# Optimization experiments

Hardware: AMD Instinct MI355X
Metric: run time of the kernel (lower is better)

Reference implementation:

```python
import jax, jax.numpy as jnp
import numpy as np

EPS = 1e-6

def rmsnorm(x, w):
    rms = jnp.sqrt(jnp.mean(x * x, axis=-1, keepdims=True) + EPS)
    return w * x / rms

def setup_inputs() -> dict:
    key = jax.random.key(0)
    ks = jax.random.split(key, 12)
    B, L, D, S, E, H = 2, 2048, 1024, 16, 4, 2048
    x = jax.random.normal(ks[0], (B, L, D), jnp.float32)
    A_log = jnp.log(jax.random.uniform(ks[1], (D, S), jnp.float32) * 0.5 + 0.5)
    D_param = jnp.ones((D,), jnp.float32)
    W_delta = jax.random.normal(ks[2], (D, D), jnp.float32) * 0.02
    b_delta = jnp.zeros((D,), jnp.float32)
    W_B = jax.random.normal(ks[3], (D, S), jnp.float32) * 0.02
    W_C = jax.random.normal(ks[4], (D, S), jnp.float32) * 0.02
    W_router = jax.random.normal(ks[5], (D, E), jnp.float32) * 0.02
    Wg = jax.random.normal(ks[6], (E, D, H), jnp.float32) * 0.02
    Wu = jax.random.normal(ks[7], (E, D, H), jnp.float32) * 0.02
    Wd = jax.random.normal(ks[8], (E, H, D), jnp.float32) * 0.02
    wn_exp = jnp.ones((E, H), jnp.float32)
    norm_w = jnp.ones((D,), jnp.float32)
    return dict(x=x, A_log=A_log, D_param=D_param, W_delta=W_delta, b_delta=b_delta,
                W_B=W_B, W_C=W_C, W_router=W_router, Wg=Wg, Wu=Wu, Wd=Wd,
                wn_exp=wn_exp, norm_w=norm_w)

def reference(x, A_log, D_param, W_delta, b_delta, W_B, W_C, W_router, Wg, Wu, Wd, wn_exp, norm_w):
    B, L, D = x.shape
    # input-dependent SSM parameters
    delta = jax.nn.softplus(x @ W_delta + b_delta)        # (B,L,D)
    Bm = x @ W_B                                          # (B,L,S)
    Cm = x @ W_C                                          # (B,L,S)
    A = -jnp.exp(A_log)                                   # (D,S)
    S = A.shape[1]
    h0 = jnp.zeros((B, D, S), x.dtype)
    xs = (jnp.moveaxis(x, 1, 0), jnp.moveaxis(delta, 1, 0),
          jnp.moveaxis(Bm, 1, 0), jnp.moveaxis(Cm, 1, 0))

    def step(h, inp):
        x_t, d_t, B_t, C_t = inp                          # (B,D),(B,D),(B,S),(B,S)
        bar_A = jnp.exp(jnp.minimum(d_t[..., None] * A, 10.0))          # (B,D,S)
        bar_B = jnp.clip(d_t[..., None] * B_t[:, None, :], -10.0, 10.0)  # (B,D,S)
        h = jnp.clip(bar_A * h + bar_B * x_t[..., None], -10000.0, 10000.0)
        y_t = jnp.sum(h * C_t[:, None, :], axis=-1) + x_t * D_param     # (B,D)
        return h, y_t

    _, ys = jax.lax.scan(step, h0, xs)                    # ys: (L,B,D)
    ssm_out = jnp.moveaxis(ys, 0, 1)                      # (B,L,D)

    # top-2 MoE over flattened tokens
    flat = ssm_out.reshape(-1, D)                         # (N,D)
    probs = jax.nn.softmax(flat @ W_router, axis=-1)      # (N,E)
    w2, idx2 = jax.lax.top_k(probs, 2)
    w2 = w2 / (jnp.sum(w2, axis=-1, keepdims=True) + 1e-9)

    def expert(xf, wg, wu, wd, wn):
        g = jax.nn.silu(xf @ wg) * (xf @ wu)
        g = rmsnorm(g, wn)
        return g @ wd

    all_out = jax.vmap(expert, in_axes=(None, 0, 0, 0, 0))(flat, Wg, Wu, Wd, wn_exp)  # (E,N,D)
    tok = jnp.arange(flat.shape[0])
    moe = (w2[:, 0, None] * all_out[idx2[:, 0], tok]
           + w2[:, 1, None] * all_out[idx2[:, 1], tok])   # (N,D)

    out = rmsnorm(ssm_out + moe.reshape(B, L, D), norm_w)
    return out  # dropout is identity in eval mode
```

## Files before the change

kernel.cpp:

```cpp
#include <hip/hip_runtime.h>
#include <hip/hip_bf16.h>


typedef __bf16 bfrag __attribute__((ext_vector_type(8)));
typedef float f32x4 __attribute__((ext_vector_type(4)));

constexpr int Ddim = 1024;
constexpr int Sdim = 16;
constexpr int Eexp = 4;
constexpr int Hdim = 2048;
constexpr int Lseq = 2048;
constexpr int Bb   = 2;
constexpr int Ntok = 4096;
constexpr int NC   = 32;
constexpr int CL   = 64;
constexpr int DG   = 64;

__device__ __forceinline__ float softplus_f(float z) {
  return z > 20.f ? z : log1pf(__expf(z));
}

__device__ __forceinline__ bfrag cvt8(float4 a, float4 b) {
  bfrag r;
  r[0] = (__bf16)a.x; r[1] = (__bf16)a.y; r[2] = (__bf16)a.z; r[3] = (__bf16)a.w;
  r[4] = (__bf16)b.x; r[5] = (__bf16)b.y; r[6] = (__bf16)b.z; r[7] = (__bf16)b.w;
  return r;
}

__device__ __forceinline__ void cvt8_split(float4 a, float4 b, bfrag& h, bfrag& l) {
  float v[8] = {a.x, a.y, a.z, a.w, b.x, b.y, b.z, b.w};
  #pragma unroll
  for (int k = 0; k < 8; k++) {
    __bf16 hh = (__bf16)v[k];
    h[k] = hh;
    l[k] = (__bf16)(v[k] - (float)hh);
  }
}

__device__ __forceinline__ void gload16(const void* g, void* l) {
  __builtin_amdgcn_global_load_lds(
      (const __attribute__((address_space(1))) void*)g,
      (__attribute__((address_space(3))) void*)l, 16, 0, 0);
}

__global__ __launch_bounds__(256) void tr_cvt(const float* __restrict__ src,
                                              __bf16* __restrict__ dst,
                                              int R, int C) {
  __shared__ float tile[32][33];
  const size_t boff = (size_t)blockIdx.z * R * C;
  const int c0 = blockIdx.x * 32, r0 = blockIdx.y * 32;
  const int tx = threadIdx.x & 31, ty = threadIdx.x >> 5;
  #pragma unroll
  for (int i = 0; i < 4; i++)
    tile[ty + 8 * i][tx] = src[boff + (size_t)(r0 + ty + 8 * i) * C + c0 + tx];
  __syncthreads();
  #pragma unroll
  for (int i = 0; i < 4; i++)
    dst[boff + (size_t)(c0 + ty + 8 * i) * R + r0 + tx] = (__bf16)tile[tx][ty + 8 * i];
}

__global__ __launch_bounds__(256) void tr_split(const float* __restrict__ src,
                                                __bf16* __restrict__ dhi,
                                                __bf16* __restrict__ dlo,
                                                int R, int C) {
  __shared__ float tile[32][33];
  const size_t boff = (size_t)blockIdx.z * R * C;
  const int c0 = blockIdx.x * 32, r0 = blockIdx.y * 32;
  const int tx = threadIdx.x & 31, ty = threadIdx.x >> 5;
  #pragma unroll
  for (int i = 0; i < 4; i++)
    tile[ty + 8 * i][tx] = src[boff + (size_t)(r0 + ty + 8 * i) * C + c0 + tx];
  __syncthreads();
  #pragma unroll
  for (int i = 0; i < 4; i++) {
    float v = tile[tx][ty + 8 * i];
    __bf16 h = (__bf16)v;
    size_t idx = boff + (size_t)(c0 + ty + 8 * i) * R + r0 + tx;
    dhi[idx] = h;
    dlo[idx] = (__bf16)(v - (float)h);
  }
}

__global__ __launch_bounds__(256) void cvt_bf(const float* __restrict__ s,
                                              __bf16* __restrict__ d) {
  const size_t i = ((size_t)blockIdx.x * 256 + threadIdx.x) * 8;
  float4 f0 = *(const float4*)&s[i];
  float4 f1 = *(const float4*)&s[i + 4];
  *(bfrag*)&d[i] = cvt8(f0, f1);
}

__global__ __launch_bounds__(256) void cvt_xsplit(const float* __restrict__ s,
                                                  __bf16* __restrict__ dh,
                                                  __bf16* __restrict__ dl) {
  const size_t i = ((size_t)blockIdx.x * 256 + threadIdx.x) * 8;
  float4 f0 = *(const float4*)&s[i];
  float4 f1 = *(const float4*)&s[i + 4];
  bfrag h, l;
  cvt8_split(f0, f1, h, l);
  *(bfrag*)&dh[i] = h;
  *(bfrag*)&dl[i] = l;
}

__global__ __launch_bounds__(256) void gemm_delta(
    const __bf16* __restrict__ xh, const __bf16* __restrict__ xl,
    const __bf16* __restrict__ Bhi, const __bf16* __restrict__ Blo,
    const float* __restrict__ bias, float* __restrict__ outp) {
  const int n0 = blockIdx.x * 128;
  const int m0 = blockIdx.y * 128;
  const int t = threadIdx.x;
  const int lane = t & 63;
  const int w = t >> 6;
  const int wm = w >> 1, wn = w & 1;
  const int lr = lane & 15, kq = lane >> 4;

  __shared__ __attribute__((aligned(16))) __bf16 Ah[128 * 32];
  __shared__ __attribute__((aligned(16))) __bf16 Al[128 * 32];
  __shared__ __attribute__((aligned(16))) __bf16 Bh[128 * 32];
  __shared__ __attribute__((aligned(16))) __bf16 Bl[128 * 32];

  f32x4 acc[4][4];
  const f32x4 z4 = {0.f, 0.f, 0.f, 0.f};
  #pragma unroll
  for (int i = 0; i < 4; i++)
    #pragma unroll
    for (int j = 0; j < 4; j++) acc[i][j] = z4;

  const int sr0 = (w * 2 + 0) * 16 + (lane >> 2);
  const int sr1 = (w * 2 + 1) * 16 + (lane >> 2);
  const int skc = (lane & 3) * 8;
  const __bf16* ah0 = xh + (size_t)(m0 + sr0) * Ddim + skc;
  const __bf16* ah1 = xh + (size_t)(m0 + sr1) * Ddim + skc;
  const __bf16* al0 = xl + (size_t)(m0 + sr0) * Ddim + skc;
  const __bf16* al1 = xl + (size_t)(m0 + sr1) * Ddim + skc;
  const __bf16* bh0 = Bhi + (size_t)(n0 + sr0) * Ddim + skc;
  const __bf16* bh1 = Bhi + (size_t)(n0 + sr1) * Ddim + skc;
  const __bf16* bl0 = Blo + (size_t)(n0 + sr0) * Ddim + skc;
  const __bf16* bl1 = Blo + (size_t)(n0 + sr1) * Ddim + skc;
  __bf16* lAh0 = &Ah[(w * 2 + 0) * 512];
  __bf16* lAh1 = &Ah[(w * 2 + 1) * 512];
  __bf16* lAl0 = &Al[(w * 2 + 0) * 512];
  __bf16* lAl1 = &Al[(w * 2 + 1) * 512];
  __bf16* lBh0 = &Bh[(w * 2 + 0) * 512];
  __bf16* lBh1 = &Bh[(w * 2 + 1) * 512];
  __bf16* lBl0 = &Bl[(w * 2 + 0) * 512];
  __bf16* lBl1 = &Bl[(w * 2 + 1) * 512];

  for (int k0 = 0; k0 < Ddim; k0 += 32) {
    __syncthreads();
    gload16(ah0 + k0, lAh0); gload16(ah1 + k0, lAh1);
    gload16(al0 + k0, lAl0); gload16(al1 + k0, lAl1);
    gload16(bh0 + k0, lBh0); gload16(bh1 + k0, lBh1);
    gload16(bl0 + k0, lBl0); gload16(bl1 + k0, lBl1);
    __syncthreads();
    bfrag ah[4], al_[4], bh[4], bl[4];
    #pragma unroll
    for (int i = 0; i < 4; i++) {
      const int off = (wm * 64 + i * 16 + lr) * 32 + kq * 8;
      ah[i] = *(const bfrag*)&Ah[off];
      al_[i] = *(const bfrag*)&Al[off];
    }
    #pragma unroll
    for (int j = 0; j < 4; j++) {
      const int off = (wn * 64 + j * 16 + lr) * 32 + kq * 8;
      bh[j] = *(const bfrag*)&Bh[off];
      bl[j] = *(const bfrag*)&Bl[off];
    }
    #pragma unroll
    for (int i = 0; i < 4; i++)
      #pragma unroll
      for (int j = 0; j < 4; j++) {
        f32x4 tacc = acc[i][j];
        tacc = __builtin_amdgcn_mfma_f32_16x16x32_bf16(al_[i], bl[j], tacc, 0, 0, 0);
        tacc = __builtin_amdgcn_mfma_f32_16x16x32_bf16(ah[i], bl[j], tacc, 0, 0, 0);
        tacc = __builtin_amdgcn_mfma_f32_16x16x32_bf16(al_[i], bh[j], tacc, 0, 0, 0);
        tacc = __builtin_amdgcn_mfma_f32_16x16x32_bf16(ah[i], bh[j], tacc, 0, 0, 0);
        acc[i][j] = tacc;
      }
  }
  #pragma unroll
  for (int i = 0; i < 4; i++)
    #pragma unroll
    for (int rr = 0; rr < 4; rr++) {
      const int row = m0 + wm * 64 + i * 16 + kq * 4 + rr;
      #pragma unroll
      for (int j = 0; j < 4; j++) {
        const int col = n0 + wn * 64 + j * 16 + lr;
        float zv = acc[i][j][rr] + bias[col];
        outp[(size_t)row * Ddim + col] = softplus_f(zv);
      }
    }
}

__global__ __launch_bounds__(256) void bc_proj(
    const float* __restrict__ x, const float* __restrict__ WB,
    const float* __restrict__ WC, float* __restrict__ Bm, float* __restrict__ Cm) {
  const int n = blockIdx.x * 4 + (threadIdx.x >> 6);
  const int lane = threadIdx.x & 63;
  const int o = lane & 31;
  const int half = lane >> 5;
  const int oc = o & 15;
  const float* W = (o < 16) ? WB : WC;
  const float* xr = x + (size_t)n * Ddim + half * 512;
  const float* Wp = W + (size_t)(half * 512) * Sdim + oc;
  float s = 0.f;
  #pragma unroll 8
  for (int k = 0; k < 512; k++) s += xr[k] * Wp[(size_t)k * Sdim];
  s += __shfl_xor(s, 32);
  if (half == 0) {
    if (o < 16) Bm[(size_t)n * Sdim + oc] = s;
    else        Cm[(size_t)n * Sdim + oc] = s;
  }
}

__global__ __launch_bounds__(1024) void scan_pass1(
    const float* __restrict__ delta, const float* __restrict__ x,
    const float* __restrict__ Bm, const float* __restrict__ A_log,
    float* __restrict__ Ac, float* __restrict__ Bc) {
  const int b = blockIdx.z, c = blockIdx.y, d0 = blockIdx.x * DG;
  const int tid = threadIdx.x;
  const int dl = tid >> 4, s = tid & 15;
  __shared__ __attribute__((aligned(16))) float ld[CL * DG];
  __shared__ __attribute__((aligned(16))) float lx[CL * DG];
  __shared__ __attribute__((aligned(16))) float lb[CL * 16];
  const int t0 = c * CL;
  {
    const int ti = tid >> 4, di = (tid & 15) * 4;
    const size_t src = ((size_t)(b * Lseq + t0 + ti)) * Ddim + d0 + di;
    *(float4*)&ld[ti * DG + di] = *(const float4*)&delta[src];
    *(float4*)&lx[ti * DG + di] = *(const float4*)&x[src];
    if (tid < 256) {
      const int tj = tid >> 2, sj = (tid & 3) * 4;
      *(float4*)&lb[tj * 16 + sj] =
          *(const float4*)&Bm[((size_t)(b * Lseq + t0 + tj)) * Sdim + sj];
    }
  }
  const float A = -__expf(A_log[(d0 + dl) * Sdim + s]);
  __syncthreads();
  float P = 1.f, S = 0.f;
  #pragma unroll 4
  for (int i = 0; i < CL; i++) {
    float dt = ld[i * DG + dl];
    float xt = lx[i * DG + dl];
    float Bt = lb[i * 16 + s];
    float a = __expf(fminf(dt * A, 10.f));
    float bb = fminf(fmaxf(dt * Bt, -10.f), 10.f);
    S = a * S + bb * xt;
    P *= a;
  }
  const size_t o = ((size_t)(b * NC + c) * Ddim + d0 + dl) * Sdim + s;
  Ac[o] = P;
  Bc[o] = S;
}

__global__ __launch_bounds__(256) void scan_pass2(float* __restrict__ Ac,
                                                  const float* __restrict__ Bc) {
  const int idx = blockIdx.x * 256 + threadIdx.x;
  const int b = idx >> 14, r = idx & 16383;
  const size_t base = (size_t)b * (NC * 16384) + r;
  float h = 0.f;
  #pragma unroll 4
  for (int c = 0; c < NC; c++) {
    const size_t a_idx = base + (size_t)c * 16384;
    float a = Ac[a_idx];
    float bb = Bc[a_idx];
    Ac[a_idx] = h;
    h = fmaf(a, h, bb);
  }
}

__global__ __launch_bounds__(1024) void scan_pass3(
    const float* __restrict__ delta, const float* __restrict__ x,
    const float* __restrict__ Bm, const float* __restrict__ Cm,
    const float* __restrict__ A_log, const float* __restrict__ Dp,
    const float* __restrict__ hstart, float* __restrict__ ssm) {
  const int b = blockIdx.z, c = blockIdx.y, d0 = blockIdx.x * DG;
  const int tid = threadIdx.x;
  const int dl = tid >> 4, s = tid & 15;
  __shared__ __attribute__((aligned(16))) float ld[CL * DG];
  __shared__ __attribute__((aligned(16))) float lx[CL * DG];
  __shared__ __attribute__((aligned(16))) float lb[CL * 16];
  __shared__ __attribute__((aligned(16))) float lc[CL * 16];
  __shared__ __attribute__((aligned(16))) float ly[CL * DG];
  const int t0 = c * CL;
  {
    const int ti = tid >> 4, di = (tid & 15) * 4;
    const size_t src = ((size_t)(b * Lseq + t0 + ti)) * Ddim + d0 + di;
    *(float4*)&ld[ti * DG + di] = *(const float4*)&delta[src];
    *(float4*)&lx[ti * DG + di] = *(const float4*)&x[src];
    if (tid < 256) {
      const int tj = tid >> 2, sj = (tid & 3) * 4;
      *(float4*)&lb[tj * 16 + sj] =
          *(const float4*)&Bm[((size_t)(b * Lseq + t0 + tj)) * Sdim + sj];
    } else if (tid < 512) {
      const int u = tid - 256;
      const int tj = u >> 2, sj = (u & 3) * 4;
      *(float4*)&lc[tj * 16 + sj] =
          *(const float4*)&Cm[((size_t)(b * Lseq + t0 + tj)) * Sdim + sj];
    }
  }
  const float A = -__expf(A_log[(d0 + dl) * Sdim + s]);
  const float Dpar = Dp[d0 + dl];
  float h = hstart[((size_t)(b * NC + c) * Ddim + d0 + dl) * Sdim + s];
  __syncthreads();
  #pragma unroll 2
  for (int i = 0; i < CL; i++) {
    float dt = ld[i * DG + dl];
    float xt = lx[i * DG + dl];
    float Bt = lb[i * 16 + s];
    float Ct = lc[i * 16 + s];
    float a = __expf(fminf(dt * A, 10.f));
    float bb = fminf(fmaxf(dt * Bt, -10.f), 10.f);
    h = a * h + bb * xt;
    float yp = h * Ct;
    yp += __shfl_xor(yp, 1);
    yp += __shfl_xor(yp, 2);
    yp += __shfl_xor(yp, 4);
    yp += __shfl_xor(yp, 8);
    if (s == 0) ly[i * DG + dl] = yp + xt * Dpar;
  }
  __syncthreads();
  {
    const int ti = tid >> 4, di = (tid & 15) * 4;
    *(float4*)&ssm[((size_t)(b * Lseq + t0 + ti)) * Ddim + d0 + di] =
        *(const float4*)&ly[ti * DG + di];
  }
}

__global__ __launch_bounds__(256) void router_k(
    const float* __restrict__ ssm, const float* __restrict__ Wr,
    int* __restrict__ counts, int* __restrict__ slotTok,
    int* __restrict__ tokSlot, float* __restrict__ tokW) {
  const int n = blockIdx.x * 4 + (threadIdx.x >> 6);
  const int lane = threadIdx.x & 63;
  const float* xr = ssm + (size_t)n * Ddim;
  float p0 = 0.f, p1 = 0.f, p2 = 0.f, p3 = 0.f;
  for (int k = lane; k < Ddim; k += 64) {
    float xv = xr[k];
    float4 wr = *(const float4*)&Wr[k * 4];
    p0 += xv * wr.x; p1 += xv * wr.y; p2 += xv * wr.z; p3 += xv * wr.w;
  }
  #pragma unroll
  for (int o = 32; o > 0; o >>= 1) {
    p0 += __shfl_xor(p0, o);
    p1 += __shfl_xor(p1, o);
    p2 += __shfl_xor(p2, o);
    p3 += __shfl_xor(p3, o);
  }
  if (lane == 0) {
    float l[4] = {p0, p1, p2, p3};
    float mx = fmaxf(fmaxf(l[0], l[1]), fmaxf(l[2], l[3]));
    float pe[4]; float sum = 0.f;
    #pragma unroll
    for (int e = 0; e < 4; e++) { pe[e] = __expf(l[e] - mx); sum += pe[e]; }
    int i0 = 0;
    #pragma unroll
    for (int e = 1; e < 4; e++) if (pe[e] > pe[i0]) i0 = e;
    int i1 = (i0 == 0) ? 1 : 0;
    #pragma unroll
    for (int e = 0; e < 4; e++) if (e != i0 && e != i1 && pe[e] > pe[i1]) i1 = e;
    float w0 = pe[i0] / sum, w1 = pe[i1] / sum;
    float dn = w0 + w1 + 1e-9f;
    w0 /= dn; w1 /= dn;
    int s0 = atomicAdd(&counts[i0], 1);
    slotTok[i0 * Ntok + s0] = n;
    tokSlot[2 * n] = i0 * Ntok + s0;
    tokW[2 * n] = w0;
    int s1 = atomicAdd(&counts[i1], 1);
    slotTok[i1 * Ntok + s1] = n;
    tokSlot[2 * n + 1] = i1 * Ntok + s1;
    tokW[2 * n + 1] = w1;
  }
}

__global__ void offs_k(const int* __restrict__ counts, int* __restrict__ offs) {
  if (threadIdx.x == 0 && blockIdx.x == 0) {
    int a = 0;
    for (int e = 0; e < Eexp; e++) { offs[e] = a; a += counts[e]; }
    offs[Eexp] = a;
  }
}

__global__ __launch_bounds__(256) void gemm_gateup(
    const __bf16* __restrict__ ssmB, const __bf16* __restrict__ WgT,
    const __bf16* __restrict__ WuT, const int* __restrict__ slotTok,
    const int* __restrict__ counts, const int* __restrict__ offs,
    __bf16* __restrict__ g) {
  const int e = blockIdx.z;
  const int cnt = counts[e];
  const int r0 = blockIdx.y * 128;
  if (r0 >= cnt) return;
  const int n0 = blockIdx.x * 128;
  const int t = threadIdx.x;
  const int lane = t & 63;
  const int w = t >> 6;
  const int wm = w >> 1, wn = w & 1;
  const int lr = lane & 15, kq = lane >> 4;

  __shared__ __attribute__((aligned(16))) __bf16 As[128 * 32];
  __shared__ __attribute__((aligned(16))) __bf16 Bgs[128 * 32];
  __shared__ __attribute__((aligned(16))) __bf16 Bus[128 * 32];

  f32x4 accG[4][4], accU[4][4];
  const f32x4 z4 = {0.f, 0.f, 0.f, 0.f};
  #pragma unroll
  for (int i = 0; i < 4; i++)
    #pragma unroll
    for (int j = 0; j < 4; j++) { accG[i][j] = z4; accU[i][j] = z4; }

  const int sr0 = (w * 2 + 0) * 16 + (lane >> 2);
  const int sr1 = (w * 2 + 1) * 16 + (lane >> 2);
  const int skc = (lane & 3) * 8;
  const int ra0 = (r0 + sr0 < cnt) ? (r0 + sr0) : (cnt - 1);
  const int ra1 = (r0 + sr1 < cnt) ? (r0 + sr1) : (cnt - 1);
  const __bf16* a0 = ssmB + (size_t)slotTok[e * Ntok + ra0] * Ddim + skc;
  const __bf16* a1 = ssmB + (size_t)slotTok[e * Ntok + ra1] * Ddim + skc;
  const size_t wb = (size_t)e * Hdim * Ddim;
  const __bf16* bg0 = WgT + wb + (size_t)(n0 + sr0) * Ddim + skc;
  const __bf16* bg1 = WgT + wb + (size_t)(n0 + sr1) * Ddim + skc;
  const __bf16* bu0 = WuT + wb + (size_t)(n0 + sr0) * Ddim + skc;
  const __bf16* bu1 = WuT + wb + (size_t)(n0 + sr1) * Ddim + skc;
  __bf16* lA0 = &As[(w * 2 + 0) * 512];
  __bf16* lA1 = &As[(w * 2 + 1) * 512];
  __bf16* lBg0 = &Bgs[(w * 2 + 0) * 512];
  __bf16* lBg1 = &Bgs[(w * 2 + 1) * 512];
  __bf16* lBu0 = &Bus[(w * 2 + 0) * 512];
  __bf16* lBu1 = &Bus[(w * 2 + 1) * 512];

  for (int k0 = 0; k0 < Ddim; k0 += 32) {
    __syncthreads();
    gload16(a0 + k0, lA0);  gload16(a1 + k0, lA1);
    gload16(bg0 + k0, lBg0); gload16(bg1 + k0, lBg1);
    gload16(bu0 + k0, lBu0); gload16(bu1 + k0, lBu1);
    __syncthreads();
    bfrag af[4], bg[4], bu[4];
    #pragma unroll
    for (int i = 0; i < 4; i++)
      af[i] = *(const bfrag*)&As[(wm * 64 + i * 16 + lr) * 32 + kq * 8];
    #pragma unroll
    for (int j = 0; j < 4; j++) {
      const int off = (wn * 64 + j * 16 + lr) * 32 + kq * 8;
      bg[j] = *(const bfrag*)&Bgs[off];
      bu[j] = *(const bfrag*)&Bus[off];
    }
    #pragma unroll
    for (int i = 0; i < 4; i++)
      #pragma unroll
      for (int j = 0; j < 4; j++) {
        accG[i][j] = __builtin_amdgcn_mfma_f32_16x16x32_bf16(af[i], bg[j], accG[i][j], 0, 0, 0);
        accU[i][j] = __builtin_amdgcn_mfma_f32_16x16x32_bf16(af[i], bu[j], accU[i][j], 0, 0, 0);
      }
  }
  const int gb = offs[e];
  #pragma unroll
  for (int i = 0; i < 4; i++)
    #pragma unroll
    for (int rr = 0; rr < 4; rr++) {
      const int r = r0 + wm * 64 + i * 16 + kq * 4 + rr;
      if (r < cnt) {
        const size_t base = (size_t)(gb + r) * Hdim + n0 + wn * 64 + lr;
        #pragma unroll
        for (int j = 0; j < 4; j++) {
          float zg = accG[i][j][rr];
          float zu = accU[i][j][rr];
          float val = zg / (1.f + __expf(-zg)) * zu;
          g[base + j * 16] = (__bf16)val;
        }
      }
    }
}

__global__ __launch_bounds__(256) void rms_g(__bf16* __restrict__ g,
                                             const float* __restrict__ wn,
                                             const int* __restrict__ offs) {
  const int gs = blockIdx.x;
  const int e = (gs >= offs[1]) + (gs >= offs[2]) + (gs >= offs[3]);
  __bf16* row = g + (size_t)gs * Hdim;
  const int t = threadIdx.x;
  bfrag v = *(const bfrag*)&row[t * 8];
  float f[8]; float ss = 0.f;
  #pragma unroll
  for (int k = 0; k < 8; k++) { f[k] = (float)v[k]; ss += f[k] * f[k]; }
  #pragma unroll
  for (int o = 32; o > 0; o >>= 1) ss += __shfl_xor(ss, o);
  __shared__ float red[4];
  if ((t & 63) == 0) red[t >> 6] = ss;
  __syncthreads();
  float tot = red[0] + red[1] + red[2] + red[3];
  float rinv = 1.f / sqrtf(tot * (1.f / Hdim) + 1e-6f);
  const float* wrow = wn + (size_t)e * Hdim + t * 8;
  bfrag o8;
  #pragma unroll
  for (int k = 0; k < 8; k++) o8[k] = (__bf16)(wrow[k] * f[k] * rinv);
  *(bfrag*)&row[t * 8] = o8;
}

__global__ __launch_bounds__(256) void gemm_down(
    const __bf16* __restrict__ g, const __bf16* __restrict__ WdT,
    const int* __restrict__ counts, const int* __restrict__ offs,
    float* __restrict__ dout) {
  const int e = blockIdx.z;
  const int cnt = counts[e];
  const int r0 = blockIdx.y * 128;
  if (r0 >= cnt) return;
  const int n0 = blockIdx.x * 128;
  const int t = threadIdx.x;
  const int lane = t & 63;
  const int w = t >> 6;
  const int wm = w >> 1, wn = w & 1;
  const int lr = lane & 15, kq = lane >> 4;

  __shared__ __attribute__((aligned(16))) __bf16 As[128 * 32];
  __shared__ __attribute__((aligned(16))) __bf16 Bs[128 * 32];

  f32x4 acc[4][4];
  const f32x4 z4 = {0.f, 0.f, 0.f, 0.f};
  #pragma unroll
  for (int i = 0; i < 4; i++)
    #pragma unroll
    for (int j = 0; j < 4; j++) acc[i][j] = z4;

  const int sr0 = (w * 2 + 0) * 16 + (lane >> 2);
  const int sr1 = (w * 2 + 1) * 16 + (lane >> 2);
  const int skc = (lane & 3) * 8;
  const int gb = offs[e];
  const int ra0 = (r0 + sr0 < cnt) ? (r0 + sr0) : (cnt - 1);
  const int ra1 = (r0 + sr1 < cnt) ? (r0 + sr1) : (cnt - 1);
  const __bf16* a0 = g + (size_t)(gb + ra0) * Hdim + skc;
  const __bf16* a1 = g + (size_t)(gb + ra1) * Hdim + skc;
  const size_t wb = (size_t)e * Ddim * Hdim;
  const __bf16* b0 = WdT + wb + (size_t)(n0 + sr0) * Hdim + skc;
  const __bf16* b1 = WdT + wb + (size_t)(n0 + sr1) * Hdim + skc;
  __bf16* lA0 = &As[(w * 2 + 0) * 512];
  __bf16* lA1 = &As[(w * 2 + 1) * 512];
  __bf16* lB0 = &Bs[(w * 2 + 0) * 512];
  __bf16* lB1 = &Bs[(w * 2 + 1) * 512];

  for (int k0 = 0; k0 < Hdim; k0 += 32) {
    __syncthreads();
    gload16(a0 + k0, lA0); gload16(a1 + k0, lA1);
    gload16(b0 + k0, lB0); gload16(b1 + k0, lB1);
    __syncthreads();
    bfrag af[4], bf_[4];
    #pragma unroll
    for (int i = 0; i < 4; i++)
      af[i] = *(const bfrag*)&As[(wm * 64 + i * 16 + lr) * 32 + kq * 8];
    #pragma unroll
    for (int j = 0; j < 4; j++)
      bf_[j] = *(const bfrag*)&Bs[(wn * 64 + j * 16 + lr) * 32 + kq * 8];
    #pragma unroll
    for (int i = 0; i < 4; i++)
      #pragma unroll
      for (int j = 0; j < 4; j++)
        acc[i][j] = __builtin_amdgcn_mfma_f32_16x16x32_bf16(af[i], bf_[j], acc[i][j], 0, 0, 0);
  }
  #pragma unroll
  for (int i = 0; i < 4; i++)
    #pragma unroll
    for (int rr = 0; rr < 4; rr++) {
      const int r = r0 + wm * 64 + i * 16 + kq * 4 + rr;
      if (r < cnt) {
        const size_t base = (size_t)(gb + r) * Ddim + n0 + wn * 64 + lr;
        #pragma unroll
        for (int j = 0; j < 4; j++)
          dout[base + j * 16] = acc[i][j][rr];
      }
    }
}

__global__ __launch_bounds__(256) void final_norm(
    const float* __restrict__ ssm, const float* __restrict__ dout,
    const int* __restrict__ tokSlot, const float* __restrict__ tokW,
    const int* __restrict__ offs, const float* __restrict__ nw,
    float* __restrict__ outp) {
  const int n = blockIdx.x;
  const int t = threadIdx.x;
  __shared__ int rows[2];
  __shared__ float ws[2];
  if (t < 2) {
    int pk = tokSlot[2 * n + t];
    rows[t] = offs[pk >> 12] + (pk & (Ntok - 1));
    ws[t] = tokW[2 * n + t];
  }
  __syncthreads();
  const int r0 = rows[0], r1 = rows[1];
  const float w0 = ws[0], w1 = ws[1];
  const size_t base = (size_t)n * Ddim + t * 4;
  float4 a = *(const float4*)&ssm[base];
  float4 m0 = *(const float4*)&dout[(size_t)r0 * Ddim + t * 4];
  float4 m1 = *(const float4*)&dout[(size_t)r1 * Ddim + t * 4];
  float v0 = a.x + w0 * m0.x + w1 * m1.x;
  float v1 = a.y + w0 * m0.y + w1 * m1.y;
  float v2 = a.z + w0 * m0.z + w1 * m1.z;
  float v3 = a.w + w0 * m0.w + w1 * m1.w;
  float ss = v0 * v0 + v1 * v1 + v2 * v2 + v3 * v3;
  #pragma unroll
  for (int o = 32; o > 0; o >>= 1) ss += __shfl_xor(ss, o);
  __shared__ float red[4];
  if ((t & 63) == 0) red[t >> 6] = ss;
  __syncthreads();
  float tot = red[0] + red[1] + red[2] + red[3];
  float rinv = 1.f / sqrtf(tot * (1.f / Ddim) + 1e-6f);
  float4 wv = *(const float4*)&nw[t * 4];
  float4 r;
  r.x = wv.x * v0 * rinv;
  r.y = wv.y * v1 * rinv;
  r.z = wv.z * v2 * rinv;
  r.w = wv.w * v3 * rinv;
  *(float4*)&outp[base] = r;
}

extern "C" void kernel_launch(void* const* d_in, const int* in_sizes, int n_in,
                              void* d_out, int out_size, void* d_ws, size_t ws_size,
                              hipStream_t stream) {
  (void)in_sizes; (void)n_in; (void)out_size; (void)ws_size;
  const float* x        = (const float*)d_in[0];
  const float* A_log    = (const float*)d_in[1];
  const float* D_param  = (const float*)d_in[2];
  const float* W_delta  = (const float*)d_in[3];
  const float* b_delta  = (const float*)d_in[4];
  const float* W_B      = (const float*)d_in[5];
  const float* W_C      = (const float*)d_in[6];
  const float* W_router = (const float*)d_in[7];
  const float* Wg       = (const float*)d_in[8];
  const float* Wu       = (const float*)d_in[9];
  const float* Wd       = (const float*)d_in[10];
  const float* wn_exp   = (const float*)d_in[11];
  const float* norm_w   = (const float*)d_in[12];
  float* out = (float*)d_out;

  char* p = (char*)d_ws;
  auto carve = [&](size_t bytes) -> void* {
    void* r = (void*)p;
    p += (bytes + 255) & ~(size_t)255;
    return r;
  };
  float*  delta   = (float*)  carve((size_t)Ntok * Ddim * 4);
  float*  Ac      = (float*)  carve((size_t)Bb * NC * Ddim * Sdim * 4);
  float*  Bc      = (float*)  carve((size_t)Bb * NC * Ddim * Sdim * 4);
  __bf16* WdT_hi  = (__bf16*) carve((size_t)Ddim * Ddim * 2);
  __bf16* WdT_lo  = (__bf16*) carve((size_t)Ddim * Ddim * 2);
  __bf16* WgT     = (__bf16*) carve((size_t)Eexp * Hdim * Ddim * 2);
  float*  dout    = delta;
  __bf16* WuT     = (__bf16*) carve((size_t)Eexp * Hdim * Ddim * 2);
  __bf16* WdnT    = (__bf16*) carve((size_t)Eexp * Ddim * Hdim * 2);
  float*  Bm      = (float*)  carve((size_t)Ntok * Sdim * 4);
  float*  Cm      = (float*)  carve((size_t)Ntok * Sdim * 4);
  float*  ssm     = (float*)  carve((size_t)Ntok * Ddim * 4);
  __bf16* gbuf    = (__bf16*) carve((size_t)2 * Ntok * Hdim * 2);
  int*    counts  = (int*)    carve(64);
  int*    offs    = (int*)    carve(64);
  int*    slotTok = (int*)    carve((size_t)Eexp * Ntok * 4);
  int*    tokSlot = (int*)    carve((size_t)2 * Ntok * 4);
  float*  tokW    = (float*)  carve((size_t)2 * Ntok * 4);

  __bf16* xh   = (__bf16*)Ac;
  __bf16* xl   = (__bf16*)gbuf;
  __bf16* ssmB = (__bf16*)delta;

  hipMemsetAsync(counts, 0, 64, stream);

  tr_split<<<dim3(Ddim / 32, Ddim / 32, 1), 256, 0, stream>>>(W_delta, WdT_hi, WdT_lo, Ddim, Ddim);
  tr_cvt<<<dim3(Hdim / 32, Ddim / 32, Eexp), 256, 0, stream>>>(Wg, WgT, Ddim, Hdim);
  tr_cvt<<<dim3(Hdim / 32, Ddim / 32, Eexp), 256, 0, stream>>>(Wu, WuT, Ddim, Hdim);
  tr_cvt<<<dim3(Ddim / 32, Hdim / 32, Eexp), 256, 0, stream>>>(Wd, WdnT, Hdim, Ddim);

  cvt_xsplit<<<Ntok * Ddim / 2048, 256, 0, stream>>>(x, xh, xl);
  gemm_delta<<<dim3(Ddim / 128, Ntok / 128), 256, 0, stream>>>(xh, xl, WdT_hi, WdT_lo, b_delta, delta);
  bc_proj<<<Ntok / 4, 256, 0, stream>>>(x, W_B, W_C, Bm, Cm);

  scan_pass1<<<dim3(Ddim / DG, NC, Bb), 1024, 0, stream>>>(delta, x, Bm, A_log, Ac, Bc);
  scan_pass2<<<Bb * Ddim * Sdim / 256, 256, 0, stream>>>(Ac, Bc);
  scan_pass3<<<dim3(Ddim / DG, NC, Bb), 1024, 0, stream>>>(delta, x, Bm, Cm, A_log, D_param, Ac, ssm);

  cvt_bf<<<Ntok * Ddim / 2048, 256, 0, stream>>>(ssm, ssmB);
  router_k<<<Ntok / 4, 256, 0, stream>>>(ssm, W_router, counts, slotTok, tokSlot, tokW);
  offs_k<<<1, 64, 0, stream>>>(counts, offs);
  gemm_gateup<<<dim3(Hdim / 128, Ntok / 128, Eexp), 256, 0, stream>>>(ssmB, WgT, WuT, slotTok, counts, offs, gbuf);
  rms_g<<<2 * Ntok, 256, 0, stream>>>(gbuf, wn_exp, offs);
  gemm_down<<<dim3(Ddim / 128, Ntok / 128, Eexp), 256, 0, stream>>>(gbuf, WdnT, counts, offs, dout);
  final_norm<<<Ntok, 256, 0, stream>>>(ssm, dout, tokSlot, tokW, offs, norm_w, out);
}
```

Measured before the change: 789.5 us.

## Double-buffer LDS tiles in delta, gate-up and down GEMMs

Each of the three MFMA GEMM kernels now holds two shared-memory buffers per operand. The next k-slice is staged into the spare buffer while the current one feeds the MFMAs, which drops one of the two barriers per iteration. The aim is to hide global-load latency behind matrix compute. The cost is doubled LDS use per block, which may lower occupancy, and the overlap only helps if gload16 is asynchronous or the compiler schedules it early.

```diff
diff --git a/kernel.cpp b/kernel.cpp
--- a/kernel.cpp
+++ b/kernel.cpp
@@ -113,10 +113,10 @@
   const int wm = w >> 1, wn = w & 1;
   const int lr = lane & 15, kq = lane >> 4;
 
-  __shared__ __attribute__((aligned(16))) __bf16 Ah[128 * 32];
-  __shared__ __attribute__((aligned(16))) __bf16 Al[128 * 32];
-  __shared__ __attribute__((aligned(16))) __bf16 Bh[128 * 32];
-  __shared__ __attribute__((aligned(16))) __bf16 Bl[128 * 32];
+  __shared__ __attribute__((aligned(16))) __bf16 Ah[2][128 * 32];
+  __shared__ __attribute__((aligned(16))) __bf16 Al[2][128 * 32];
+  __shared__ __attribute__((aligned(16))) __bf16 Bh[2][128 * 32];
+  __shared__ __attribute__((aligned(16))) __bf16 Bl[2][128 * 32];
 
   f32x4 acc[4][4];
   const f32x4 z4 = {0.f, 0.f, 0.f, 0.f};
@@ -136,34 +136,33 @@
   const __bf16* bh1 = Bhi + (size_t)(n0 + sr1) * Ddim + skc;
   const __bf16* bl0 = Blo + (size_t)(n0 + sr0) * Ddim + skc;
   const __bf16* bl1 = Blo + (size_t)(n0 + sr1) * Ddim + skc;
-  __bf16* lAh0 = &Ah[(w * 2 + 0) * 512];
-  __bf16* lAh1 = &Ah[(w * 2 + 1) * 512];
-  __bf16* lAl0 = &Al[(w * 2 + 0) * 512];
-  __bf16* lAl1 = &Al[(w * 2 + 1) * 512];
-  __bf16* lBh0 = &Bh[(w * 2 + 0) * 512];
-  __bf16* lBh1 = &Bh[(w * 2 + 1) * 512];
-  __bf16* lBl0 = &Bl[(w * 2 + 0) * 512];
-  __bf16* lBl1 = &Bl[(w * 2 + 1) * 512];
-
+  const int c0 = (w * 2 + 0) * 512;
+  const int c1 = (w * 2 + 1) * 512;
+
+  auto stg = [&](int bf, int k0) {
+    gload16(ah0 + k0, &Ah[bf][c0]); gload16(ah1 + k0, &Ah[bf][c1]);
+    gload16(al0 + k0, &Al[bf][c0]); gload16(al1 + k0, &Al[bf][c1]);
+    gload16(bh0 + k0, &Bh[bf][c0]); gload16(bh1 + k0, &Bh[bf][c1]);
+    gload16(bl0 + k0, &Bl[bf][c0]); gload16(bl1 + k0, &Bl[bf][c1]);
+  };
+
+  stg(0, 0);
+  __syncthreads();
   for (int k0 = 0; k0 < Ddim; k0 += 32) {
-    __syncthreads();
-    gload16(ah0 + k0, lAh0); gload16(ah1 + k0, lAh1);
-    gload16(al0 + k0, lAl0); gload16(al1 + k0, lAl1);
-    gload16(bh0 + k0, lBh0); gload16(bh1 + k0, lBh1);
-    gload16(bl0 + k0, lBl0); gload16(bl1 + k0, lBl1);
-    __syncthreads();
+    const int cur = (k0 >> 5) & 1;
+    if (k0 + 32 < Ddim) stg(cur ^ 1, k0 + 32);
     bfrag ah[4], al_[4], bh[4], bl[4];
     #pragma unroll
     for (int i = 0; i < 4; i++) {
       const int off = (wm * 64 + i * 16 + lr) * 32 + kq * 8;
-      ah[i] = *(const bfrag*)&Ah[off];
-      al_[i] = *(const bfrag*)&Al[off];
+      ah[i] = *(const bfrag*)&Ah[cur][off];
+      al_[i] = *(const bfrag*)&Al[cur][off];
     }
     #pragma unroll
     for (int j = 0; j < 4; j++) {
       const int off = (wn * 64 + j * 16 + lr) * 32 + kq * 8;
-      bh[j] = *(const bfrag*)&Bh[off];
-      bl[j] = *(const bfrag*)&Bl[off];
+      bh[j] = *(const bfrag*)&Bh[cur][off];
+      bl[j] = *(const bfrag*)&Bl[cur][off];
     }
     #pragma unroll
     for (int i = 0; i < 4; i++)
@@ -176,6 +175,7 @@
         tacc = __builtin_amdgcn_mfma_f32_16x16x32_bf16(ah[i], bh[j], tacc, 0, 0, 0);
         acc[i][j] = tacc;
       }
+    __syncthreads();
   }
   #pragma unroll
   for (int i = 0; i < 4; i++)
@@ -396,9 +396,9 @@
   const int wm = w >> 1, wn = w & 1;
   const int lr = lane & 15, kq = lane >> 4;
 
-  __shared__ __attribute__((aligned(16))) __bf16 As[128 * 32];
-  __shared__ __attribute__((aligned(16))) __bf16 Bgs[128 * 32];
-  __shared__ __attribute__((aligned(16))) __bf16 Bus[128 * 32];
+  __shared__ __attribute__((aligned(16))) __bf16 As[2][128 * 32];
+  __shared__ __attribute__((aligned(16))) __bf16 Bgs[2][128 * 32];
+  __shared__ __attribute__((aligned(16))) __bf16 Bus[2][128 * 32];
 
   f32x4 accG[4][4], accU[4][4];
   const f32x4 z4 = {0.f, 0.f, 0.f, 0.f};
@@ -419,28 +419,29 @@
   const __bf16* bg1 = WgT + wb + (size_t)(n0 + sr1) * Ddim + skc;
   const __bf16* bu0 = WuT + wb + (size_t)(n0 + sr0) * Ddim + skc;
   const __bf16* bu1 = WuT + wb + (size_t)(n0 + sr1) * Ddim + skc;
-  __bf16* lA0 = &As[(w * 2 + 0) * 512];
-  __bf16* lA1 = &As[(w * 2 + 1) * 512];
-  __bf16* lBg0 = &Bgs[(w * 2 + 0) * 512];
-  __bf16* lBg1 = &Bgs[(w * 2 + 1) * 512];
-  __bf16* lBu0 = &Bus[(w * 2 + 0) * 512];
-  __bf16* lBu1 = &Bus[(w * 2 + 1) * 512];
-
+  const int c0 = (w * 2 + 0) * 512;
+  const int c1 = (w * 2 + 1) * 512;
+
+  auto stg = [&](int bf, int k0) {
+    gload16(a0 + k0, &As[bf][c0]);   gload16(a1 + k0, &As[bf][c1]);
+    gload16(bg0 + k0, &Bgs[bf][c0]); gload16(bg1 + k0, &Bgs[bf][c1]);
+    gload16(bu0 + k0, &Bus[bf][c0]); gload16(bu1 + k0, &Bus[bf][c1]);
+  };
+
+  stg(0, 0);
+  __syncthreads();
   for (int k0 = 0; k0 < Ddim; k0 += 32) {
-    __syncthreads();
-    gload16(a0 + k0, lA0);  gload16(a1 + k0, lA1);
-    gload16(bg0 + k0, lBg0); gload16(bg1 + k0, lBg1);
-    gload16(bu0 + k0, lBu0); gload16(bu1 + k0, lBu1);
-    __syncthreads();
+    const int cur = (k0 >> 5) & 1;
+    if (k0 + 32 < Ddim) stg(cur ^ 1, k0 + 32);
     bfrag af[4], bg[4], bu[4];
     #pragma unroll
     for (int i = 0; i < 4; i++)
-      af[i] = *(const bfrag*)&As[(wm * 64 + i * 16 + lr) * 32 + kq * 8];
+      af[i] = *(const bfrag*)&As[cur][(wm * 64 + i * 16 + lr) * 32 + kq * 8];
     #pragma unroll
     for (int j = 0; j < 4; j++) {
       const int off = (wn * 64 + j * 16 + lr) * 32 + kq * 8;
-      bg[j] = *(const bfrag*)&Bgs[off];
-      bu[j] = *(const bfrag*)&Bus[off];
+      bg[j] = *(const bfrag*)&Bgs[cur][off];
+      bu[j] = *(const bfrag*)&Bus[cur][off];
     }
     #pragma unroll
     for (int i = 0; i < 4; i++)
@@ -449,6 +450,7 @@
         accG[i][j] = __builtin_amdgcn_mfma_f32_16x16x32_bf16(af[i], bg[j], accG[i][j], 0, 0, 0);
         accU[i][j] = __builtin_amdgcn_mfma_f32_16x16x32_bf16(af[i], bu[j], accU[i][j], 0, 0, 0);
       }
+    __syncthreads();
   }
   const int gb = offs[e];
   #pragma unroll
@@ -509,8 +511,8 @@
   const int wm = w >> 1, wn = w & 1;
   const int lr = lane & 15, kq = lane >> 4;
 
-  __shared__ __attribute__((aligned(16))) __bf16 As[128 * 32];
-  __shared__ __attribute__((aligned(16))) __bf16 Bs[128 * 32];
+  __shared__ __attribute__((aligned(16))) __bf16 As[2][128 * 32];
+  __shared__ __attribute__((aligned(16))) __bf16 Bs[2][128 * 32];
 
   f32x4 acc[4][4];
   const f32x4 z4 = {0.f, 0.f, 0.f, 0.f};
@@ -530,28 +532,32 @@
   const size_t wb = (size_t)e * Ddim * Hdim;
   const __bf16* b0 = WdT + wb + (size_t)(n0 + sr0) * Hdim + skc;
   const __bf16* b1 = WdT + wb + (size_t)(n0 + sr1) * Hdim + skc;
-  __bf16* lA0 = &As[(w * 2 + 0) * 512];
-  __bf16* lA1 = &As[(w * 2 + 1) * 512];
-  __bf16* lB0 = &Bs[(w * 2 + 0) * 512];
-  __bf16* lB1 = &Bs[(w * 2 + 1) * 512];
-
+  const int c0 = (w * 2 + 0) * 512;
+  const int c1 = (w * 2 + 1) * 512;
+
+  auto stg = [&](int bf, int k0) {
+    gload16(a0 + k0, &As[bf][c0]); gload16(a1 + k0, &As[bf][c1]);
+    gload16(b0 + k0, &Bs[bf][c0]); gload16(b1 + k0, &Bs[bf][c1]);
+  };
+
+  stg(0, 0);
+  __syncthreads();
   for (int k0 = 0; k0 < Hdim; k0 += 32) {
-    __syncthreads();
-    gload16(a0 + k0, lA0); gload16(a1 + k0, lA1);
-    gload16(b0 + k0, lB0); gload16(b1 + k0, lB1);
-    __syncthreads();
+    const int cur = (k0 >> 5) & 1;
+    if (k0 + 32 < Hdim) stg(cur ^ 1, k0 + 32);
     bfrag af[4], bf_[4];
     #pragma unroll
     for (int i = 0; i < 4; i++)
-      af[i] = *(const bfrag*)&As[(wm * 64 + i * 16 + lr) * 32 + kq * 8];
+      af[i] = *(const bfrag*)&As[cur][(wm * 64 + i * 16 + lr) * 32 + kq * 8];
     #pragma unroll
     for (int j = 0; j < 4; j++)
-      bf_[j] = *(const bfrag*)&Bs[(wn * 64 + j * 16 + lr) * 32 + kq * 8];
+      bf_[j] = *(const bfrag*)&Bs[cur][(wn * 64 + j * 16 + lr) * 32 + kq * 8];
     #pragma unroll
     for (int i = 0; i < 4; i++)
       #pragma unroll
       for (int j = 0; j < 4; j++)
         acc[i][j] = __builtin_amdgcn_mfma_f32_16x16x32_bf16(af[i], bf_[j], acc[i][j], 0, 0, 0);
+    __syncthreads();
   }
   #pragma unroll
   for (int i = 0; i < 4; i++)
```

Result: faster. 736.5 us (-6.7%).
